# Performance work log

Hardware: AMD Instinct MI355X
Metric: run time of the kernel (lower is better)

Reference implementation:

```python
import jax, jax.numpy as jnp
import numpy as np

B, T, IN, H, OUT = 16384, 200, 9, 64, 3


def setup_inputs() -> dict:
    key = jax.random.key(0)
    ks = jax.random.split(key, 12)
    s_in, s_h = 1.0 / np.sqrt(H), 1.0 / np.sqrt(H)  # torch LSTMCell init scale = 1/sqrt(hidden)
    u = lambda k, shape: jax.random.uniform(k, shape, jnp.float32, -s_h, s_h)
    return {
        "x": jax.random.normal(ks[0], (B, T, IN), jnp.float32),
        "W_ih1": u(ks[1], (4 * H, IN)),
        "W_hh1": u(ks[2], (4 * H, H)),
        "b_ih1": u(ks[3], (4 * H,)),
        "b_hh1": u(ks[4], (4 * H,)),
        "W_ih2": u(ks[5], (4 * H, H)),
        "W_hh2": u(ks[6], (4 * H, H)),
        "b_ih2": u(ks[7], (4 * H,)),
        "b_hh2": u(ks[8], (4 * H,)),
        "W_out": u(ks[9], (OUT, H)),
        "b_out": u(ks[10], (OUT,)),
    }


def _lstm_cell(x, h, c, W_ih, W_hh, b_ih, b_hh):
    # PyTorch gate order: i, f, g, o
    gates = x @ W_ih.T + b_ih + h @ W_hh.T + b_hh  # [B, 4H]
    i, f, g, o = jnp.split(gates, 4, axis=-1)
    i, f, o = jax.nn.sigmoid(i), jax.nn.sigmoid(f), jax.nn.sigmoid(o)
    g = jnp.tanh(g)
    c_new = f * c + i * g
    h_new = o * jnp.tanh(c_new)
    return h_new, c_new


def reference(x, W_ih1, W_hh1, b_ih1, b_hh1, W_ih2, W_hh2, b_ih2, b_hh2, W_out, b_out):
    batch = x.shape[0]
    hdim = W_hh1.shape[1]
    zeros = jnp.zeros((batch, hdim), x.dtype)
    init = (zeros, zeros, zeros, zeros)  # h1, c1, h2, c2

    def step(carry, x_t):
        h1, c1, h2, c2 = carry
        h1, c1 = _lstm_cell(x_t, h1, c1, W_ih1, W_hh1, b_ih1, b_hh1)
        h2, c2 = _lstm_cell(h1, h2, c2, W_ih2, W_hh2, b_ih2, b_hh2)
        return (h1, c1, h2, c2), None

    (h1, c1, h2, c2), _ = jax.lax.scan(step, init, jnp.swapaxes(x, 0, 1))  # scan over time
    out = h2 @ W_out.T + b_out  # [B, OUT]
    return out[:, None, :]  # [B, 1, OUT]
```

## Files before the change

### kernel.cpp

```cpp
#include <hip/hip_runtime.h>
#include <hip/hip_bf16.h>


#define B_TOT   16384
#define T_STEPS 200
#define IN_DIM  9
#define HDIM    64

#define PK1_OFF 0
#define PK2_OFF 24576
#define BSUM_HALF_OFF 57344
#define PACK_W_TOT 57344
#define PACK_TOT (PACK_W_TOT + 512)

#define L2E      1.44269504089f
#define NEG2L2E -2.88539008178f

typedef _Float16 half8 __attribute__((ext_vector_type(8)));
typedef float    f32x4 __attribute__((ext_vector_type(4)));

__device__ __forceinline__ float sig_y(float y) {
    return __builtin_amdgcn_rcpf(1.0f + __builtin_amdgcn_exp2f(y));
}

__global__ void pack_kernel(const float* __restrict__ Wih1, const float* __restrict__ Whh1,
                            const float* __restrict__ bih1, const float* __restrict__ bhh1,
                            const float* __restrict__ Wih2, const float* __restrict__ Whh2,
                            const float* __restrict__ bih2, const float* __restrict__ bhh2,
                            float* __restrict__ ws) {
    int e = blockIdx.x * 256 + threadIdx.x;
    if (e >= PACK_TOT) return;
    _Float16* wh = (_Float16*)ws;
    float* bptr = (float*)(wh + BSUM_HALF_OFF);
    auto gscale = [](int q) -> float {
        int gt = q >> 6;
        return (gt == 2) ? (2.0f * L2E) : -L2E;
    };
    if (e < PK2_OFF) {
        int j = e & 7, lane = (e >> 3) & 63, nt = (e >> 9) & 15, c = e >> 13;
        int k = c * 32 + 4 * (lane >> 4) + (j & 3) + 16 * (j >> 2);
        int q = nt * 16 + (lane & 15);
        float v = 0.0f;
        if (k < 64)      v = Whh1[q * 64 + k];
        else if (k < 73) v = Wih1[q * 9 + (k - 64)];
        wh[e] = (_Float16)(v * gscale(q));
    } else if (e < PACK_W_TOT) {
        int e2 = e - PK2_OFF;
        int j = e2 & 7, lane = (e2 >> 3) & 63, nt = (e2 >> 9) & 15, c = e2 >> 13;
        int k = c * 32 + 4 * (lane >> 4) + (j & 3) + 16 * (j >> 2);
        int q = nt * 16 + (lane & 15);
        float v = (k < 64) ? Wih2[q * 64 + k] : Whh2[q * 64 + (k - 64)];
        wh[e] = (_Float16)(v * gscale(q));
    } else if (e < PACK_W_TOT + 256) {
        int q = e - PACK_W_TOT;
        bptr[q] = (bih1[q] + bhh1[q]) * gscale(q);
    } else {
        int q = e - PACK_W_TOT - 256;
        bptr[256 + q] = (bih2[q] + bhh2[q]) * gscale(q);
    }
}

__global__ __launch_bounds__(256, 1) void lstm_mfma(
    const float* __restrict__ x,
    const float* __restrict__ ws_f,
    const float* __restrict__ Wout,
    const float* __restrict__ bout,
    float* __restrict__ out)
{
    const int tid  = threadIdx.x;
    const int lane = tid & 63;
    const int w    = __builtin_amdgcn_readfirstlane(tid >> 6);
    const int l15  = lane & 15;
    const int l4   = lane >> 4;

    const _Float16* wh  = (const _Float16*)ws_f;
    const _Float16* pk1 = wh + PK1_OFF;
    const _Float16* pk2 = wh + PK2_OFF;
    const float* bsum   = (const float*)(wh + BSUM_HALF_OFF);

    __shared__ _Float16 h1s[2][16][72];
    __shared__ _Float16 h2s[2][16][72];
    __shared__ _Float16 xwin[8][16][40];

    for (int i = tid; i < 2 * 16 * 72; i += 256) {
        (&h1s[0][0][0])[i] = (_Float16)0.0f;
        (&h2s[0][0][0])[i] = (_Float16)0.0f;
    }
    for (int i = tid; i < 8 * 16 * 40; i += 256) (&xwin[0][0][0])[i] = (_Float16)0.0f;

    const int bbase = blockIdx.x * 16;

    const int wb = tid >> 4;
    const int e0 = tid & 15;
    int lw_s[5], lw_pos[5], lw_idx[5], lw_ok[5];
    #pragma unroll
    for (int r = 0; r < 5; ++r) {
        int idx = e0 + 16 * r;
        lw_ok[r]  = (idx < 72);
        int s = idx / 9, k = idx - s * 9;
        lw_s[r]   = s;
        lw_idx[r] = idx;
        lw_pos[r] = 8 * (k >> 2) + (k & 3);
    }
    const float* xb = x + (long)(bbase + wb) * (T_STEPS * IN_DIM);

    auto load_window = [&](int wbase) {
        float v[5];
        #pragma unroll
        for (int r = 0; r < 5; ++r)
            if (lw_ok[r]) v[r] = xb[wbase * IN_DIM + lw_idx[r]];
        #pragma unroll
        for (int r = 0; r < 5; ++r)
            if (lw_ok[r]) xwin[lw_s[r]][wb][lw_pos[r]] = (_Float16)v[r];
    };
    __syncthreads();
    load_window(0);

    half8 bw1_00, bw1_01, bw1_02, bw1_03;
    half8 bw1_10, bw1_11, bw1_12, bw1_13;
    half8 bw1_20, bw1_21, bw1_22, bw1_23;
    half8 bw2_00, bw2_01, bw2_02, bw2_03;
    half8 bw2_10, bw2_11, bw2_12, bw2_13;
    half8 bw2_20, bw2_21, bw2_22, bw2_23;
    half8 bw2_30, bw2_31, bw2_32, bw2_33;
    {
        #define LD1(c,g) *(const half8*)(pk1 + (((c * 16) + (w + 4 * g)) * 64 + lane) * 8)
        #define LD2(c,g) *(const half8*)(pk2 + (((c * 16) + (w + 4 * g)) * 64 + lane) * 8)
        bw1_00 = LD1(0,0); bw1_01 = LD1(0,1); bw1_02 = LD1(0,2); bw1_03 = LD1(0,3);
        bw1_10 = LD1(1,0); bw1_11 = LD1(1,1); bw1_12 = LD1(1,2); bw1_13 = LD1(1,3);
        bw1_20 = LD1(2,0); bw1_21 = LD1(2,1); bw1_22 = LD1(2,2); bw1_23 = LD1(2,3);
        bw2_00 = LD2(0,0); bw2_01 = LD2(0,1); bw2_02 = LD2(0,2); bw2_03 = LD2(0,3);
        bw2_10 = LD2(1,0); bw2_11 = LD2(1,1); bw2_12 = LD2(1,2); bw2_13 = LD2(1,3);
        bw2_20 = LD2(2,0); bw2_21 = LD2(2,1); bw2_22 = LD2(2,2); bw2_23 = LD2(2,3);
        bw2_30 = LD2(3,0); bw2_31 = LD2(3,1); bw2_32 = LD2(3,2); bw2_33 = LD2(3,3);
        #undef LD1
        #undef LD2
    }

    float bias1[4], bias2[4];
    #pragma unroll
    for (int g = 0; g < 4; ++g) {
        bias1[g] = bsum[(w + 4 * g) * 16 + l15];
        bias2[g] = bsum[256 + (w + 4 * g) * 16 + l15];
    }

    const int hpos = ((w >> 1) << 5) + 8 * (l15 >> 2) + (l15 & 3) + ((w & 1) << 2);

    f32x4 c1 = {0.f, 0.f, 0.f, 0.f};
    f32x4 c2 = {0.f, 0.f, 0.f, 0.f};

    __syncthreads();

    int p = 0;
    for (int t = 0; t < T_STEPS; ++t) {
        const int ts = t & 7;

        asm volatile("" :
            "+v"(bw1_00), "+v"(bw1_01), "+v"(bw1_02), "+v"(bw1_03),
            "+v"(bw1_10), "+v"(bw1_11), "+v"(bw1_12), "+v"(bw1_13),
            "+v"(bw1_20), "+v"(bw1_21), "+v"(bw1_22), "+v"(bw1_23));
        asm volatile("" :
            "+v"(bw2_00), "+v"(bw2_01), "+v"(bw2_02), "+v"(bw2_03),
            "+v"(bw2_10), "+v"(bw2_11), "+v"(bw2_12), "+v"(bw2_13),
            "+v"(bw2_20), "+v"(bw2_21), "+v"(bw2_22), "+v"(bw2_23),
            "+v"(bw2_30), "+v"(bw2_31), "+v"(bw2_32), "+v"(bw2_33),
            "+v"(bias1[0]), "+v"(bias1[1]), "+v"(bias1[2]), "+v"(bias1[3]),
            "+v"(bias2[0]), "+v"(bias2[1]), "+v"(bias2[2]), "+v"(bias2[3]));

        half8 a1c0 = *(const half8*)&h1s[p][l15][ 0 + 8 * l4];
        half8 a1c1 = *(const half8*)&h1s[p][l15][32 + 8 * l4];
        half8 a2h0 = *(const half8*)&h2s[p][l15][ 0 + 8 * l4];
        half8 a2h1 = *(const half8*)&h2s[p][l15][32 + 8 * l4];
        half8 ax   = *(const half8*)&xwin[ts][l15][8 * l4];

        f32x4 C[4];
        #pragma unroll
        for (int g = 0; g < 4; ++g) C[g] = (f32x4){bias1[g], bias1[g], bias1[g], bias1[g]};
        C[0] = __builtin_amdgcn_mfma_f32_16x16x32_f16(a1c0, bw1_00, C[0], 0, 0, 0);
        C[1] = __builtin_amdgcn_mfma_f32_16x16x32_f16(a1c0, bw1_01, C[1], 0, 0, 0);
        C[2] = __builtin_amdgcn_mfma_f32_16x16x32_f16(a1c0, bw1_02, C[2], 0, 0, 0);
        C[3] = __builtin_amdgcn_mfma_f32_16x16x32_f16(a1c0, bw1_03, C[3], 0, 0, 0);
        C[0] = __builtin_amdgcn_mfma_f32_16x16x32_f16(a1c1, bw1_10, C[0], 0, 0, 0);
        C[1] = __builtin_amdgcn_mfma_f32_16x16x32_f16(a1c1, bw1_11, C[1], 0, 0, 0);
        C[2] = __builtin_amdgcn_mfma_f32_16x16x32_f16(a1c1, bw1_12, C[2], 0, 0, 0);
        C[3] = __builtin_amdgcn_mfma_f32_16x16x32_f16(a1c1, bw1_13, C[3], 0, 0, 0);
        C[0] = __builtin_amdgcn_mfma_f32_16x16x32_f16(ax,   bw1_20, C[0], 0, 0, 0);
        C[1] = __builtin_amdgcn_mfma_f32_16x16x32_f16(ax,   bw1_21, C[1], 0, 0, 0);
        C[2] = __builtin_amdgcn_mfma_f32_16x16x32_f16(ax,   bw1_22, C[2], 0, 0, 0);
        C[3] = __builtin_amdgcn_mfma_f32_16x16x32_f16(ax,   bw1_23, C[3], 0, 0, 0);

        f32x4 D[4];
        #pragma unroll
        for (int g = 0; g < 4; ++g) D[g] = (f32x4){bias2[g], bias2[g], bias2[g], bias2[g]};
        D[0] = __builtin_amdgcn_mfma_f32_16x16x32_f16(a2h0, bw2_20, D[0], 0, 0, 0);
        D[1] = __builtin_amdgcn_mfma_f32_16x16x32_f16(a2h0, bw2_21, D[1], 0, 0, 0);
        D[2] = __builtin_amdgcn_mfma_f32_16x16x32_f16(a2h0, bw2_22, D[2], 0, 0, 0);
        D[3] = __builtin_amdgcn_mfma_f32_16x16x32_f16(a2h0, bw2_23, D[3], 0, 0, 0);
        D[0] = __builtin_amdgcn_mfma_f32_16x16x32_f16(a2h1, bw2_30, D[0], 0, 0, 0);
        D[1] = __builtin_amdgcn_mfma_f32_16x16x32_f16(a2h1, bw2_31, D[1], 0, 0, 0);
        D[2] = __builtin_amdgcn_mfma_f32_16x16x32_f16(a2h1, bw2_32, D[2], 0, 0, 0);
        D[3] = __builtin_amdgcn_mfma_f32_16x16x32_f16(a2h1, bw2_33, D[3], 0, 0, 0);

        #pragma unroll
        for (int r = 0; r < 4; ++r) {
            float ig = sig_y(C[0][r]);
            float fg = sig_y(C[1][r]);
            float gg = __builtin_fmaf(-2.0f, sig_y(C[2][r]), 1.0f);
            float og = sig_y(C[3][r]);
            float cc = __builtin_fmaf(fg, c1[r], ig * gg);
            c1[r] = cc;
            float th = __builtin_fmaf(2.0f, sig_y(cc * NEG2L2E), -1.0f);
            h1s[1 - p][4 * l4 + r][hpos] = (_Float16)(og * th);
        }
        __syncthreads();

        if (ts == 7 && t + 1 < T_STEPS) load_window(t + 1);

        half8 a20 = *(const half8*)&h1s[1 - p][l15][ 0 + 8 * l4];
        half8 a21 = *(const half8*)&h1s[1 - p][l15][32 + 8 * l4];
        D[0] = __builtin_amdgcn_mfma_f32_16x16x32_f16(a20, bw2_00, D[0], 0, 0, 0);
        D[1] = __builtin_amdgcn_mfma_f32_16x16x32_f16(a20, bw2_01, D[1], 0, 0, 0);
        D[2] = __builtin_amdgcn_mfma_f32_16x16x32_f16(a20, bw2_02, D[2], 0, 0, 0);
        D[3] = __builtin_amdgcn_mfma_f32_16x16x32_f16(a20, bw2_03, D[3], 0, 0, 0);
        D[0] = __builtin_amdgcn_mfma_f32_16x16x32_f16(a21, bw2_10, D[0], 0, 0, 0);
        D[1] = __builtin_amdgcn_mfma_f32_16x16x32_f16(a21, bw2_11, D[1], 0, 0, 0);
        D[2] = __builtin_amdgcn_mfma_f32_16x16x32_f16(a21, bw2_12, D[2], 0, 0, 0);
        D[3] = __builtin_amdgcn_mfma_f32_16x16x32_f16(a21, bw2_13, D[3], 0, 0, 0);

        #pragma unroll
        for (int r = 0; r < 4; ++r) {
            float ig = sig_y(D[0][r]);
            float fg = sig_y(D[1][r]);
            float gg = __builtin_fmaf(-2.0f, sig_y(D[2][r]), 1.0f);
            float og = sig_y(D[3][r]);
            float cc = __builtin_fmaf(fg, c2[r], ig * gg);
            c2[r] = cc;
            float th = __builtin_fmaf(2.0f, sig_y(cc * NEG2L2E), -1.0f);
            h2s[1 - p][4 * l4 + r][hpos] = (_Float16)(og * th);
        }
        __syncthreads();
        p ^= 1;
    }

    if (tid < 48) {
        int bl = tid / 3, o = tid - bl * 3;
        float acc = bout[o];
        #pragma unroll 8
        for (int pos = 0; pos < HDIM; ++pos) {
            int sub = pos & 31;
            int j = (pos >> 5) * 32 + (((sub >> 2) & 1) << 4) + ((sub >> 3) << 2) + (sub & 3);
            acc = __builtin_fmaf(Wout[o * 64 + j], (float)h2s[p][bl][pos], acc);
        }
        out[(bbase + bl) * 3 + o] = acc;
    }
}

extern "C" void kernel_launch(void* const* d_in, const int* in_sizes, int n_in,
                              void* d_out, int out_size, void* d_ws, size_t ws_size,
                              hipStream_t stream) {
    const float* x     = (const float*)d_in[0];
    const float* Wih1  = (const float*)d_in[1];
    const float* Whh1  = (const float*)d_in[2];
    const float* bih1  = (const float*)d_in[3];
    const float* bhh1  = (const float*)d_in[4];
    const float* Wih2  = (const float*)d_in[5];
    const float* Whh2  = (const float*)d_in[6];
    const float* bih2  = (const float*)d_in[7];
    const float* bhh2  = (const float*)d_in[8];
    const float* Wout  = (const float*)d_in[9];
    const float* bout  = (const float*)d_in[10];
    float* ws  = (float*)d_ws;
    float* out = (float*)d_out;

    pack_kernel<<<(PACK_TOT + 255) / 256, 256, 0, stream>>>(
        Wih1, Whh1, bih1, bhh1, Wih2, Whh2, bih2, bhh2, ws);

    lstm_mfma<<<B_TOT / 16, 256, 0, stream>>>(x, ws, Wout, bout, out);
}
```

Before: 609.1 us.

## Replace transcendental gate activations with LDS lookup tables and register-stream x

Swaps the exp2/rcp-based sigmoid and tanh for linearly interpolated lookup tables of 1024 entries each. The tables are built in the pack kernel and copied into shared memory per block, and the gate weights and biases are prescaled and offset to give table indices directly. The shared-memory x window is replaced by per-lane register prefetch of the next timestep's input. This trades transcendental ALU work for LDS gathers and clamping, and adds interpolation error plus saturation outside the table range (about ±16 for sigmoid and ±8 for tanh).

```diff
diff --git a/kernel.cpp b/kernel.cpp
--- a/kernel.cpp
+++ b/kernel.cpp
@@ -9,19 +9,15 @@
 
 #define PK1_OFF 0
 #define PK2_OFF 24576
+#define PACK_W_TOT 57344
 #define BSUM_HALF_OFF 57344
-#define PACK_W_TOT 57344
 #define PACK_TOT (PACK_W_TOT + 512)
-
-#define L2E      1.44269504089f
-#define NEG2L2E -2.88539008178f
+#define TAB_BYTE_OFF (57344*2 + 512*4)
+#define N_TAB_E 2048
 
 typedef _Float16 half8 __attribute__((ext_vector_type(8)));
 typedef float    f32x4 __attribute__((ext_vector_type(4)));
-
-__device__ __forceinline__ float sig_y(float y) {
-    return __builtin_amdgcn_rcpf(1.0f + __builtin_amdgcn_exp2f(y));
-}
+typedef float    f4u   __attribute__((ext_vector_type(4), aligned(4)));
 
 __global__ void pack_kernel(const float* __restrict__ Wih1, const float* __restrict__ Whh1,
                             const float* __restrict__ bih1, const float* __restrict__ bhh1,
@@ -29,12 +25,13 @@
                             const float* __restrict__ bih2, const float* __restrict__ bhh2,
                             float* __restrict__ ws) {
     int e = blockIdx.x * 256 + threadIdx.x;
-    if (e >= PACK_TOT) return;
+    if (e >= PACK_TOT + N_TAB_E) return;
     _Float16* wh = (_Float16*)ws;
     float* bptr = (float*)(wh + BSUM_HALF_OFF);
+    float2* sigt = (float2*)((char*)ws + TAB_BYTE_OFF);
+    float2* tant = sigt + 1024;
     auto gscale = [](int q) -> float {
-        int gt = q >> 6;
-        return (gt == 2) ? (2.0f * L2E) : -L2E;
+        return ((q >> 6) == 2) ? 64.0f : 32.0f;
     };
     if (e < PK2_OFF) {
         int j = e & 7, lane = (e >> 3) & 63, nt = (e >> 9) & 15, c = e >> 13;
@@ -53,10 +50,26 @@
         wh[e] = (_Float16)(v * gscale(q));
     } else if (e < PACK_W_TOT + 256) {
         int q = e - PACK_W_TOT;
-        bptr[q] = (bih1[q] + bhh1[q]) * gscale(q);
+        bptr[q] = (bih1[q] + bhh1[q]) * gscale(q) + 512.0f;
+    } else if (e < PACK_TOT) {
+        int q = e - PACK_W_TOT - 256;
+        bptr[256 + q] = (bih2[q] + bhh2[q]) * gscale(q) + 512.0f;
     } else {
-        int q = e - PACK_W_TOT - 256;
-        bptr[256 + q] = (bih2[q] + bhh2[q]) * gscale(q);
+        int j = e - PACK_TOT;
+        if (j < 1024) {
+            float x0 = (j - 512) * (1.0f / 32.0f);
+            float x1 = (j - 511) * (1.0f / 32.0f);
+            float a = 1.0f / (1.0f + __expf(-x0));
+            float b = 1.0f / (1.0f + __expf(-x1));
+            sigt[j] = make_float2(a, b - a);
+        } else {
+            int j2 = j - 1024;
+            float y0 = (j2 - 512) * (1.0f / 64.0f);
+            float y1 = (j2 - 511) * (1.0f / 64.0f);
+            float a = tanhf(y0);
+            float b = tanhf(y1);
+            tant[j2] = make_float2(a, b - a);
+        }
     }
 }
 
@@ -80,41 +93,28 @@
 
     __shared__ _Float16 h1s[2][16][72];
     __shared__ _Float16 h2s[2][16][72];
-    __shared__ _Float16 xwin[8][16][40];
-
+    __shared__ float2 sigt[1024];
+    __shared__ float2 tant[1024];
+
+    {
+        const float2* gsig = (const float2*)((const char*)ws_f + TAB_BYTE_OFF);
+        for (int i = tid; i < 1024; i += 256) {
+            sigt[i] = gsig[i];
+            tant[i] = gsig[1024 + i];
+        }
+    }
     for (int i = tid; i < 2 * 16 * 72; i += 256) {
         (&h1s[0][0][0])[i] = (_Float16)0.0f;
         (&h2s[0][0][0])[i] = (_Float16)0.0f;
     }
-    for (int i = tid; i < 8 * 16 * 40; i += 256) (&xwin[0][0][0])[i] = (_Float16)0.0f;
 
     const int bbase = blockIdx.x * 16;
-
-    const int wb = tid >> 4;
-    const int e0 = tid & 15;
-    int lw_s[5], lw_pos[5], lw_idx[5], lw_ok[5];
-    #pragma unroll
-    for (int r = 0; r < 5; ++r) {
-        int idx = e0 + 16 * r;
-        lw_ok[r]  = (idx < 72);
-        int s = idx / 9, k = idx - s * 9;
-        lw_s[r]   = s;
-        lw_idx[r] = idx;
-        lw_pos[r] = 8 * (k >> 2) + (k & 3);
-    }
-    const float* xb = x + (long)(bbase + wb) * (T_STEPS * IN_DIM);
-
-    auto load_window = [&](int wbase) {
-        float v[5];
-        #pragma unroll
-        for (int r = 0; r < 5; ++r)
-            if (lw_ok[r]) v[r] = xb[wbase * IN_DIM + lw_idx[r]];
-        #pragma unroll
-        for (int r = 0; r < 5; ++r)
-            if (lw_ok[r]) xwin[lw_s[r]][wb][lw_pos[r]] = (_Float16)v[r];
-    };
-    __syncthreads();
-    load_window(0);
+    const float* xb = x + (long)(bbase + l15) * (T_STEPS * IN_DIM);
+
+    f4u  cx  = {0.f, 0.f, 0.f, 0.f};
+    float cx8 = 0.0f;
+    if (l4 < 2)       cx  = *(const f4u*)(xb + 4 * l4);
+    else if (l4 == 2) cx8 = xb[8];
 
     half8 bw1_00, bw1_01, bw1_02, bw1_03;
     half8 bw1_10, bw1_11, bw1_12, bw1_13;
@@ -149,12 +149,18 @@
     f32x4 c1 = {0.f, 0.f, 0.f, 0.f};
     f32x4 c2 = {0.f, 0.f, 0.f, 0.f};
 
+    auto lut = [&](const float2* t, float u) -> float {
+        float uc = __builtin_fminf(__builtin_fmaxf(u, 0.0f), 1022.999f);
+        int idx = (int)uc;
+        float fr = uc - (float)idx;
+        float2 en = t[idx];
+        return __builtin_fmaf(fr, en.y, en.x);
+    };
+
     __syncthreads();
 
     int p = 0;
     for (int t = 0; t < T_STEPS; ++t) {
-        const int ts = t & 7;
-
         asm volatile("" :
             "+v"(bw1_00), "+v"(bw1_01), "+v"(bw1_02), "+v"(bw1_03),
             "+v"(bw1_10), "+v"(bw1_11), "+v"(bw1_12), "+v"(bw1_13),
@@ -163,15 +169,25 @@
             "+v"(bw2_00), "+v"(bw2_01), "+v"(bw2_02), "+v"(bw2_03),
             "+v"(bw2_10), "+v"(bw2_11), "+v"(bw2_12), "+v"(bw2_13),
             "+v"(bw2_20), "+v"(bw2_21), "+v"(bw2_22), "+v"(bw2_23),
-            "+v"(bw2_30), "+v"(bw2_31), "+v"(bw2_32), "+v"(bw2_33),
-            "+v"(bias1[0]), "+v"(bias1[1]), "+v"(bias1[2]), "+v"(bias1[3]),
-            "+v"(bias2[0]), "+v"(bias2[1]), "+v"(bias2[2]), "+v"(bias2[3]));
+            "+v"(bw2_30), "+v"(bw2_31), "+v"(bw2_32), "+v"(bw2_33));
+
+        half8 ax;
+        {
+            float e0 = (l4 == 2) ? cx8 : cx[0];
+            ax[0] = (_Float16)e0;    ax[1] = (_Float16)cx[1];
+            ax[2] = (_Float16)cx[2]; ax[3] = (_Float16)cx[3];
+            ax[4] = ax[5] = ax[6] = ax[7] = (_Float16)0.0f;
+            if (t + 1 < T_STEPS) {
+                const float* xp = xb + (t + 1) * IN_DIM;
+                if (l4 < 2)       cx  = *(const f4u*)(xp + 4 * l4);
+                else if (l4 == 2) cx8 = xp[8];
+            }
+        }
 
         half8 a1c0 = *(const half8*)&h1s[p][l15][ 0 + 8 * l4];
         half8 a1c1 = *(const half8*)&h1s[p][l15][32 + 8 * l4];
         half8 a2h0 = *(const half8*)&h2s[p][l15][ 0 + 8 * l4];
         half8 a2h1 = *(const half8*)&h2s[p][l15][32 + 8 * l4];
-        half8 ax   = *(const half8*)&xwin[ts][l15][8 * l4];
 
         f32x4 C[4];
         #pragma unroll
@@ -203,18 +219,16 @@
 
         #pragma unroll
         for (int r = 0; r < 4; ++r) {
-            float ig = sig_y(C[0][r]);
-            float fg = sig_y(C[1][r]);
-            float gg = __builtin_fmaf(-2.0f, sig_y(C[2][r]), 1.0f);
-            float og = sig_y(C[3][r]);
+            float ig = lut(sigt, C[0][r]);
+            float fg = lut(sigt, C[1][r]);
+            float gg = lut(tant, C[2][r]);
+            float og = lut(sigt, C[3][r]);
             float cc = __builtin_fmaf(fg, c1[r], ig * gg);
             c1[r] = cc;
-            float th = __builtin_fmaf(2.0f, sig_y(cc * NEG2L2E), -1.0f);
+            float th = lut(tant, __builtin_fmaf(cc, 64.0f, 512.0f));
             h1s[1 - p][4 * l4 + r][hpos] = (_Float16)(og * th);
         }
         __syncthreads();
-
-        if (ts == 7 && t + 1 < T_STEPS) load_window(t + 1);
 
         half8 a20 = *(const half8*)&h1s[1 - p][l15][ 0 + 8 * l4];
         half8 a21 = *(const half8*)&h1s[1 - p][l15][32 + 8 * l4];
@@ -229,13 +243,13 @@
 
         #pragma unroll
         for (int r = 0; r < 4; ++r) {
-            float ig = sig_y(D[0][r]);
-            float fg = sig_y(D[1][r]);
-            float gg = __builtin_fmaf(-2.0f, sig_y(D[2][r]), 1.0f);
-            float og = sig_y(D[3][r]);
+            float ig = lut(sigt, D[0][r]);
+            float fg = lut(sigt, D[1][r]);
+            float gg = lut(tant, D[2][r]);
+            float og = lut(sigt, D[3][r]);
             float cc = __builtin_fmaf(fg, c2[r], ig * gg);
             c2[r] = cc;
-            float th = __builtin_fmaf(2.0f, sig_y(cc * NEG2L2E), -1.0f);
+            float th = lut(tant, __builtin_fmaf(cc, 64.0f, 512.0f));
             h2s[1 - p][4 * l4 + r][hpos] = (_Float16)(og * th);
         }
         __syncthreads();
@@ -249,7 +263,7 @@
         for (int pos = 0; pos < HDIM; ++pos) {
             int sub = pos & 31;
             int j = (pos >> 5) * 32 + (((sub >> 2) & 1) << 4) + ((sub >> 3) << 2) + (sub & 3);
-            acc = __builtin_fmaf(Wout[o * 64 + j], (float)h2s[p][bl][pos], acc);
+            acc = __builtin_fmaf(Wout[o * 64 + j], (float)h2s[0][bl][pos], acc);
         }
         out[(bbase + bl) * 3 + o] = acc;
     }
@@ -272,7 +286,7 @@
     float* ws  = (float*)d_ws;
     float* out = (float*)d_out;
 
-    pack_kernel<<<(PACK_TOT + 255) / 256, 256, 0, stream>>>(
+    pack_kernel<<<(PACK_TOT + N_TAB_E + 255) / 256, 256, 0, stream>>>(
         Wih1, Whh1, bih1, bhh1, Wih2, Whh2, bih2, bhh2, ws);
 
     lstm_mfma<<<B_TOT / 16, 256, 0, stream>>>(x, ws, Wout, bout, out);
```

New measurement: 811.5 us. +33.2%, slower.

## Software-pipeline LSTM layers with one barrier per step and fused gate math

Applied to the files above, without the earlier changes.

Restructures the time loop so that layer-1 gates for step t+1 are computed right after layer-2's matmuls for step t. This leaves one __syncthreads per timestep instead of two. x is now read directly into registers with a two-step prefetch instead of through an LDS window, and the gate nonlinearities are merged into a shared-denominator form with fewer reciprocals. Launch bounds are raised to two blocks per CU to improve occupancy. The costs are higher register pressure and a trickier hazard: h2s is read at step t and written at the end of the same step without a barrier in between, which relies on double-buffer parity.

```diff
diff --git a/kernel.cpp b/kernel.cpp
--- a/kernel.cpp
+++ b/kernel.cpp
@@ -13,15 +13,12 @@
 #define PACK_W_TOT 57344
 #define PACK_TOT (PACK_W_TOT + 512)
 
-#define L2E      1.44269504089f
-#define NEG2L2E -2.88539008178f
+#define L2E     1.44269504089f
+#define TWOL2E  2.88539008178f
 
 typedef _Float16 half8 __attribute__((ext_vector_type(8)));
 typedef float    f32x4 __attribute__((ext_vector_type(4)));
-
-__device__ __forceinline__ float sig_y(float y) {
-    return __builtin_amdgcn_rcpf(1.0f + __builtin_amdgcn_exp2f(y));
-}
+typedef float    f4u   __attribute__((ext_vector_type(4), aligned(4)));
 
 __global__ void pack_kernel(const float* __restrict__ Wih1, const float* __restrict__ Whh1,
                             const float* __restrict__ bih1, const float* __restrict__ bhh1,
@@ -34,7 +31,7 @@
     float* bptr = (float*)(wh + BSUM_HALF_OFF);
     auto gscale = [](int q) -> float {
         int gt = q >> 6;
-        return (gt == 2) ? (2.0f * L2E) : -L2E;
+        return (gt == 2) ? (-2.0f * L2E) : -L2E;
     };
     if (e < PK2_OFF) {
         int j = e & 7, lane = (e >> 3) & 63, nt = (e >> 9) & 15, c = e >> 13;
@@ -60,7 +57,7 @@
     }
 }
 
-__global__ __launch_bounds__(256, 1) void lstm_mfma(
+__global__ __launch_bounds__(256, 2) void lstm_mfma(
     const float* __restrict__ x,
     const float* __restrict__ ws_f,
     const float* __restrict__ Wout,
@@ -80,41 +77,31 @@
 
     __shared__ _Float16 h1s[2][16][72];
     __shared__ _Float16 h2s[2][16][72];
-    __shared__ _Float16 xwin[8][16][40];
 
     for (int i = tid; i < 2 * 16 * 72; i += 256) {
         (&h1s[0][0][0])[i] = (_Float16)0.0f;
         (&h2s[0][0][0])[i] = (_Float16)0.0f;
     }
-    for (int i = tid; i < 8 * 16 * 40; i += 256) (&xwin[0][0][0])[i] = (_Float16)0.0f;
+    __syncthreads();
 
     const int bbase = blockIdx.x * 16;
-
-    const int wb = tid >> 4;
-    const int e0 = tid & 15;
-    int lw_s[5], lw_pos[5], lw_idx[5], lw_ok[5];
-    #pragma unroll
-    for (int r = 0; r < 5; ++r) {
-        int idx = e0 + 16 * r;
-        lw_ok[r]  = (idx < 72);
-        int s = idx / 9, k = idx - s * 9;
-        lw_s[r]   = s;
-        lw_idx[r] = idx;
-        lw_pos[r] = 8 * (k >> 2) + (k & 3);
-    }
-    const float* xb = x + (long)(bbase + wb) * (T_STEPS * IN_DIM);
-
-    auto load_window = [&](int wbase) {
-        float v[5];
-        #pragma unroll
-        for (int r = 0; r < 5; ++r)
-            if (lw_ok[r]) v[r] = xb[wbase * IN_DIM + lw_idx[r]];
-        #pragma unroll
-        for (int r = 0; r < 5; ++r)
-            if (lw_ok[r]) xwin[lw_s[r]][wb][lw_pos[r]] = (_Float16)v[r];
-    };
-    __syncthreads();
-    load_window(0);
+    const float* xb = x + (long)(bbase + l15) * (T_STEPS * IN_DIM);
+
+    f4u  cx  = {0.f, 0.f, 0.f, 0.f};
+    float cx8 = 0.0f;
+    auto prefetch_x = [&](int tt) {
+        const float* xp = xb + tt * IN_DIM;
+        if (l4 < 2)       cx  = *(const f4u*)(xp + 4 * l4);
+        else if (l4 == 2) cx8 = xp[8];
+    };
+    auto build_ax = [&]() -> half8 {
+        half8 ax;
+        float e0 = (l4 == 2) ? cx8 : cx[0];
+        ax[0] = (_Float16)e0;    ax[1] = (_Float16)cx[1];
+        ax[2] = (_Float16)cx[2]; ax[3] = (_Float16)cx[3];
+        ax[4] = ax[5] = ax[6] = ax[7] = (_Float16)0.0f;
+        return ax;
+    };
 
     half8 bw1_00, bw1_01, bw1_02, bw1_03;
     half8 bw1_10, bw1_11, bw1_12, bw1_13;
@@ -149,12 +136,46 @@
     f32x4 c1 = {0.f, 0.f, 0.f, 0.f};
     f32x4 c2 = {0.f, 0.f, 0.f, 0.f};
 
-    __syncthreads();
+    auto cell_update = [&](f32x4* G, f32x4& cs, _Float16* hb) {
+        #pragma unroll
+        for (int r = 0; r < 4; ++r) {
+            float ei = __builtin_amdgcn_exp2f(G[0][r]);
+            float ef = __builtin_amdgcn_exp2f(G[1][r]);
+            float eg = __builtin_amdgcn_exp2f(G[2][r]);
+            float eo = __builtin_amdgcn_exp2f(G[3][r]);
+            float ai = 1.0f + ei, af = 1.0f + ef, ag = 1.0f + eg;
+            float gm = 1.0f - eg;
+            float pp = ai * ag;
+            float num = __builtin_fmaf(gm, af, cs[r] * pp);
+            float den = af * pp;
+            float cc  = num * __builtin_amdgcn_rcpf(den);
+            cs[r] = cc;
+            float z  = cc * TWOL2E;
+            int   zi = __float_as_int(z);
+            float ec = __builtin_amdgcn_exp2f(__int_as_float(zi | (int)0x80000000));
+            float tm = 1.0f - ec;
+            float d2 = (1.0f + eo) * (1.0f + ec);
+            float hs = __int_as_float(__float_as_int(tm) ^ (zi & (int)0x80000000));
+            float hv = hs * __builtin_amdgcn_rcpf(d2);
+            hb[(4 * l4 + r) * 72 + hpos] = (_Float16)hv;
+        }
+    };
+
+    prefetch_x(0);
+    f32x4 C[4];
+    {
+        half8 ax0 = build_ax();
+        #pragma unroll
+        for (int g = 0; g < 4; ++g) C[g] = (f32x4){bias1[g], bias1[g], bias1[g], bias1[g]};
+        C[0] = __builtin_amdgcn_mfma_f32_16x16x32_f16(ax0, bw1_20, C[0], 0, 0, 0);
+        C[1] = __builtin_amdgcn_mfma_f32_16x16x32_f16(ax0, bw1_21, C[1], 0, 0, 0);
+        C[2] = __builtin_amdgcn_mfma_f32_16x16x32_f16(ax0, bw1_22, C[2], 0, 0, 0);
+        C[3] = __builtin_amdgcn_mfma_f32_16x16x32_f16(ax0, bw1_23, C[3], 0, 0, 0);
+    }
+    prefetch_x(1);
 
     int p = 0;
     for (int t = 0; t < T_STEPS; ++t) {
-        const int ts = t & 7;
-
         asm volatile("" :
             "+v"(bw1_00), "+v"(bw1_01), "+v"(bw1_02), "+v"(bw1_03),
             "+v"(bw1_10), "+v"(bw1_11), "+v"(bw1_12), "+v"(bw1_13),
@@ -167,31 +188,29 @@
             "+v"(bias1[0]), "+v"(bias1[1]), "+v"(bias1[2]), "+v"(bias1[3]),
             "+v"(bias2[0]), "+v"(bias2[1]), "+v"(bias2[2]), "+v"(bias2[3]));
 
-        half8 a1c0 = *(const half8*)&h1s[p][l15][ 0 + 8 * l4];
-        half8 a1c1 = *(const half8*)&h1s[p][l15][32 + 8 * l4];
+        cell_update(C, c1, &h1s[1 - p][0][0]);
+
+        __syncthreads();
+
+        half8 a10  = *(const half8*)&h1s[1 - p][l15][ 0 + 8 * l4];
+        half8 a11  = *(const half8*)&h1s[1 - p][l15][32 + 8 * l4];
         half8 a2h0 = *(const half8*)&h2s[p][l15][ 0 + 8 * l4];
         half8 a2h1 = *(const half8*)&h2s[p][l15][32 + 8 * l4];
-        half8 ax   = *(const half8*)&xwin[ts][l15][8 * l4];
-
-        f32x4 C[4];
-        #pragma unroll
-        for (int g = 0; g < 4; ++g) C[g] = (f32x4){bias1[g], bias1[g], bias1[g], bias1[g]};
-        C[0] = __builtin_amdgcn_mfma_f32_16x16x32_f16(a1c0, bw1_00, C[0], 0, 0, 0);
-        C[1] = __builtin_amdgcn_mfma_f32_16x16x32_f16(a1c0, bw1_01, C[1], 0, 0, 0);
-        C[2] = __builtin_amdgcn_mfma_f32_16x16x32_f16(a1c0, bw1_02, C[2], 0, 0, 0);
-        C[3] = __builtin_amdgcn_mfma_f32_16x16x32_f16(a1c0, bw1_03, C[3], 0, 0, 0);
-        C[0] = __builtin_amdgcn_mfma_f32_16x16x32_f16(a1c1, bw1_10, C[0], 0, 0, 0);
-        C[1] = __builtin_amdgcn_mfma_f32_16x16x32_f16(a1c1, bw1_11, C[1], 0, 0, 0);
-        C[2] = __builtin_amdgcn_mfma_f32_16x16x32_f16(a1c1, bw1_12, C[2], 0, 0, 0);
-        C[3] = __builtin_amdgcn_mfma_f32_16x16x32_f16(a1c1, bw1_13, C[3], 0, 0, 0);
-        C[0] = __builtin_amdgcn_mfma_f32_16x16x32_f16(ax,   bw1_20, C[0], 0, 0, 0);
-        C[1] = __builtin_amdgcn_mfma_f32_16x16x32_f16(ax,   bw1_21, C[1], 0, 0, 0);
-        C[2] = __builtin_amdgcn_mfma_f32_16x16x32_f16(ax,   bw1_22, C[2], 0, 0, 0);
-        C[3] = __builtin_amdgcn_mfma_f32_16x16x32_f16(ax,   bw1_23, C[3], 0, 0, 0);
+        half8 ax   = build_ax();
+        int nt = t + 2; if (nt > T_STEPS - 1) nt = T_STEPS - 1;
+        prefetch_x(nt);
 
         f32x4 D[4];
         #pragma unroll
         for (int g = 0; g < 4; ++g) D[g] = (f32x4){bias2[g], bias2[g], bias2[g], bias2[g]};
+        D[0] = __builtin_amdgcn_mfma_f32_16x16x32_f16(a10,  bw2_00, D[0], 0, 0, 0);
+        D[1] = __builtin_amdgcn_mfma_f32_16x16x32_f16(a10,  bw2_01, D[1], 0, 0, 0);
+        D[2] = __builtin_amdgcn_mfma_f32_16x16x32_f16(a10,  bw2_02, D[2], 0, 0, 0);
+        D[3] = __builtin_amdgcn_mfma_f32_16x16x32_f16(a10,  bw2_03, D[3], 0, 0, 0);
+        D[0] = __builtin_amdgcn_mfma_f32_16x16x32_f16(a11,  bw2_10, D[0], 0, 0, 0);
+        D[1] = __builtin_amdgcn_mfma_f32_16x16x32_f16(a11,  bw2_11, D[1], 0, 0, 0);
+        D[2] = __builtin_amdgcn_mfma_f32_16x16x32_f16(a11,  bw2_12, D[2], 0, 0, 0);
+        D[3] = __builtin_amdgcn_mfma_f32_16x16x32_f16(a11,  bw2_13, D[3], 0, 0, 0);
         D[0] = __builtin_amdgcn_mfma_f32_16x16x32_f16(a2h0, bw2_20, D[0], 0, 0, 0);
         D[1] = __builtin_amdgcn_mfma_f32_16x16x32_f16(a2h0, bw2_21, D[1], 0, 0, 0);
         D[2] = __builtin_amdgcn_mfma_f32_16x16x32_f16(a2h0, bw2_22, D[2], 0, 0, 0);
@@ -201,46 +220,29 @@
         D[2] = __builtin_amdgcn_mfma_f32_16x16x32_f16(a2h1, bw2_32, D[2], 0, 0, 0);
         D[3] = __builtin_amdgcn_mfma_f32_16x16x32_f16(a2h1, bw2_33, D[3], 0, 0, 0);
 
-        #pragma unroll
-        for (int r = 0; r < 4; ++r) {
-            float ig = sig_y(C[0][r]);
-            float fg = sig_y(C[1][r]);
-            float gg = __builtin_fmaf(-2.0f, sig_y(C[2][r]), 1.0f);
-            float og = sig_y(C[3][r]);
-            float cc = __builtin_fmaf(fg, c1[r], ig * gg);
-            c1[r] = cc;
-            float th = __builtin_fmaf(2.0f, sig_y(cc * NEG2L2E), -1.0f);
-            h1s[1 - p][4 * l4 + r][hpos] = (_Float16)(og * th);
-        }
-        __syncthreads();
-
-        if (ts == 7 && t + 1 < T_STEPS) load_window(t + 1);
-
-        half8 a20 = *(const half8*)&h1s[1 - p][l15][ 0 + 8 * l4];
-        half8 a21 = *(const half8*)&h1s[1 - p][l15][32 + 8 * l4];
-        D[0] = __builtin_amdgcn_mfma_f32_16x16x32_f16(a20, bw2_00, D[0], 0, 0, 0);
-        D[1] = __builtin_amdgcn_mfma_f32_16x16x32_f16(a20, bw2_01, D[1], 0, 0, 0);
-        D[2] = __builtin_amdgcn_mfma_f32_16x16x32_f16(a20, bw2_02, D[2], 0, 0, 0);
-        D[3] = __builtin_amdgcn_mfma_f32_16x16x32_f16(a20, bw2_03, D[3], 0, 0, 0);
-        D[0] = __builtin_amdgcn_mfma_f32_16x16x32_f16(a21, bw2_10, D[0], 0, 0, 0);
-        D[1] = __builtin_amdgcn_mfma_f32_16x16x32_f16(a21, bw2_11, D[1], 0, 0, 0);
-        D[2] = __builtin_amdgcn_mfma_f32_16x16x32_f16(a21, bw2_12, D[2], 0, 0, 0);
-        D[3] = __builtin_amdgcn_mfma_f32_16x16x32_f16(a21, bw2_13, D[3], 0, 0, 0);
-
-        #pragma unroll
-        for (int r = 0; r < 4; ++r) {
-            float ig = sig_y(D[0][r]);
-            float fg = sig_y(D[1][r]);
-            float gg = __builtin_fmaf(-2.0f, sig_y(D[2][r]), 1.0f);
-            float og = sig_y(D[3][r]);
-            float cc = __builtin_fmaf(fg, c2[r], ig * gg);
-            c2[r] = cc;
-            float th = __builtin_fmaf(2.0f, sig_y(cc * NEG2L2E), -1.0f);
-            h2s[1 - p][4 * l4 + r][hpos] = (_Float16)(og * th);
-        }
-        __syncthreads();
+        f32x4 Cn[4];
+        #pragma unroll
+        for (int g = 0; g < 4; ++g) Cn[g] = (f32x4){bias1[g], bias1[g], bias1[g], bias1[g]};
+        Cn[0] = __builtin_amdgcn_mfma_f32_16x16x32_f16(a10, bw1_00, Cn[0], 0, 0, 0);
+        Cn[1] = __builtin_amdgcn_mfma_f32_16x16x32_f16(a10, bw1_01, Cn[1], 0, 0, 0);
+        Cn[2] = __builtin_amdgcn_mfma_f32_16x16x32_f16(a10, bw1_02, Cn[2], 0, 0, 0);
+        Cn[3] = __builtin_amdgcn_mfma_f32_16x16x32_f16(a10, bw1_03, Cn[3], 0, 0, 0);
+        Cn[0] = __builtin_amdgcn_mfma_f32_16x16x32_f16(a11, bw1_10, Cn[0], 0, 0, 0);
+        Cn[1] = __builtin_amdgcn_mfma_f32_16x16x32_f16(a11, bw1_11, Cn[1], 0, 0, 0);
+        Cn[2] = __builtin_amdgcn_mfma_f32_16x16x32_f16(a11, bw1_12, Cn[2], 0, 0, 0);
+        Cn[3] = __builtin_amdgcn_mfma_f32_16x16x32_f16(a11, bw1_13, Cn[3], 0, 0, 0);
+        Cn[0] = __builtin_amdgcn_mfma_f32_16x16x32_f16(ax,  bw1_20, Cn[0], 0, 0, 0);
+        Cn[1] = __builtin_amdgcn_mfma_f32_16x16x32_f16(ax,  bw1_21, Cn[1], 0, 0, 0);
+        Cn[2] = __builtin_amdgcn_mfma_f32_16x16x32_f16(ax,  bw1_22, Cn[2], 0, 0, 0);
+        Cn[3] = __builtin_amdgcn_mfma_f32_16x16x32_f16(ax,  bw1_23, Cn[3], 0, 0, 0);
+
+        cell_update(D, c2, &h2s[1 - p][0][0]);
+
+        #pragma unroll
+        for (int g = 0; g < 4; ++g) C[g] = Cn[g];
         p ^= 1;
     }
+    __syncthreads();
 
     if (tid < 48) {
         int bl = tid / 3, o = tid - bl * 3;
@@ -249,7 +251,7 @@
         for (int pos = 0; pos < HDIM; ++pos) {
             int sub = pos & 31;
             int j = (pos >> 5) * 32 + (((sub >> 2) & 1) << 4) + ((sub >> 3) << 2) + (sub & 3);
-            acc = __builtin_fmaf(Wout[o * 64 + j], (float)h2s[p][bl][pos], acc);
+            acc = __builtin_fmaf(Wout[o * 64 + j], (float)h2s[0][bl][pos], acc);
         }
         out[(bbase + bl) * 3 + o] = acc;
     }
```

Result: no change. 597.4 us (-1.9%).
